# Optimization experiments

Hardware: AMD Instinct MI355X
Metric: run time of the kernel (lower is better)

Reference implementation:

```python
import jax, jax.numpy as jnp
import numpy as np

B, N, D = 2, 2048, 512
H, HD = 8, 64
R = 64  # graph_radius
SCALE = HD ** -0.5
LN_EPS = 1e-5


def _ln(x, g, b):
    m = jnp.mean(x, axis=-1, keepdims=True)
    v = jnp.mean((x - m) ** 2, axis=-1, keepdims=True)
    return (x - m) * jax.lax.rsqrt(v + LN_EPS) * g + b


def setup_inputs() -> dict:
    key = jax.random.key(0)
    ks = jax.random.split(key, 8)
    w = lambda k, shape: (jax.random.normal(k, shape, jnp.float32) * 0.02)
    return {
        "nodes": jax.random.normal(ks[0], (B, N, D), jnp.float32),
        "ln1_g": jnp.ones((D,), jnp.float32), "ln1_b": jnp.zeros((D,), jnp.float32),
        "qkv_w": w(ks[1], (D, 3 * D)), "qkv_b": jnp.zeros((3 * D,), jnp.float32),
        "proj_w": w(ks[2], (D, D)), "proj_b": jnp.zeros((D,), jnp.float32),
        "rep_scale": jnp.ones((H,), jnp.float32),
        "rel_bias": w(ks[3], (2 * N - 1, H)),
        "ln2_g": jnp.ones((D,), jnp.float32), "ln2_b": jnp.zeros((D,), jnp.float32),
        "mlp_w1": w(ks[4], (D, 2 * D)), "mlp_b1": jnp.zeros((2 * D,), jnp.float32),
        "mlp_w2": w(ks[5], (2 * D, D)), "mlp_b2": jnp.zeros((D,), jnp.float32),
    }


def reference(nodes, ln1_g, ln1_b, qkv_w, qkv_b, proj_w, proj_b, rep_scale,
              rel_bias, ln2_g, ln2_b, mlp_w1, mlp_b1, mlp_w2, mlp_b2):
    b, n, d = nodes.shape
    x = _ln(nodes, ln1_g, ln1_b)                       # [B,N,D]
    qkv = (x @ qkv_w + qkv_b).reshape(b, n, 3, H, HD)
    qkv = jnp.transpose(qkv, (2, 0, 3, 1, 4))          # [3,B,H,N,HD]
    q, k, v = qkv[0], qkv[1], qkv[2]
    logits = jnp.einsum('bhnd,bhmd->bhnm', q, k) * SCALE
    # representation correlation (F.normalize with eps=1e-12)
    rep = x / jnp.maximum(jnp.linalg.norm(x, axis=-1, keepdims=True), 1e-12)
    corr = jnp.einsum('bnd,bmd->bnm', rep, rep)        # [B,N,N]
    logits = logits + corr[:, None] * rep_scale[None, :, None, None]
    pos = jnp.arange(n)
    relidx = pos[:, None] - pos[None, :]               # [N,N]
    bias = rel_bias[relidx + n - 1]                    # [N,N,H]
    logits = logits + jnp.transpose(bias, (2, 0, 1))[None]
    mask = jnp.abs(relidx) <= R
    logits = jnp.where(mask[None, None], logits, -jnp.inf)
    attn = jax.nn.softmax(logits, axis=-1)
    upd = jnp.einsum('bhnm,bhmd->bnhd', attn, v).reshape(b, n, d)
    nodes = nodes + (upd @ proj_w + proj_b)
    y = _ln(nodes, ln2_g, ln2_b)
    h = jax.nn.gelu(y @ mlp_w1 + mlp_b1, approximate=False)
    return nodes + (h @ mlp_w2 + mlp_b2)
```

## Files before the change

kernel.cpp:

```cpp
#include <hip/hip_runtime.h>
#include <math.h>

typedef __bf16 bf16;
typedef __bf16 bf16x4 __attribute__((ext_vector_type(4)));
typedef __bf16 bf16x8 __attribute__((ext_vector_type(8)));
typedef float floatx4 __attribute__((ext_vector_type(4)));

#define BB 2
#define NN 2048
#define DD 512
#define HH 8
#define HD 64
#define RR 64
#define D3 1536
#define NEG_BIG (-1e30f)
#define TQ 32
#define TBAND 160

#define GL2LDS16(g, l)                                                        \
    __builtin_amdgcn_global_load_lds(                                         \
        (const __attribute__((address_space(1))) void*)(const void*)(g),      \
        (__attribute__((address_space(3))) void*)(void*)(l), 16, 0, 0)

__global__ __launch_bounds__(256) void cvt_all_kernel(
    const float* __restrict__ qkv_w, const float* __restrict__ proj_w,
    const float* __restrict__ m1w, const float* __restrict__ m2w,
    bf16* __restrict__ wqt, bf16* __restrict__ wpt,
    bf16* __restrict__ w1t, bf16* __restrict__ w2t) {
    __shared__ bf16 Ts[64][72];
    const int tid = threadIdx.x;
    int bid = blockIdx.x;
    const float* W; bf16* Wt; int K, N, bx, by;
    if (bid < 192)      { W = qkv_w;  Wt = wqt; K = 512;  N = 1536; bx = bid % 24; by = bid / 24; }
    else if (bid < 256) { bid -= 192; W = proj_w; Wt = wpt; K = 512;  N = 512;  bx = bid % 8;  by = bid / 8; }
    else if (bid < 384) { bid -= 256; W = m1w;  Wt = w1t; K = 512;  N = 1024; bx = bid % 16; by = bid / 16; }
    else                { bid -= 384; W = m2w;  Wt = w2t; K = 1024; N = 512;  bx = bid % 8;  by = bid / 8; }
    const int n0 = bx * 64, k0 = by * 64;
    #pragma unroll
    for (int i = 0; i < 4; i++) {
        int r = (tid >> 4) + i * 16;
        int c = (tid & 15) * 4;
        floatx4 v = *(const floatx4*)(W + (size_t)(k0 + r) * N + n0 + c);
        #pragma unroll
        for (int e = 0; e < 4; e++) Ts[r][c + e] = (bf16)v[e];
    }
    __syncthreads();
    #pragma unroll
    for (int i = 0; i < 4; i++) {
        int n = (tid >> 4) + i * 16;
        int k = (tid & 15) * 4;
        bf16x4 o;
        #pragma unroll
        for (int e = 0; e < 4; e++) o[e] = Ts[k + e][n];
        *(bf16x4*)(Wt + (size_t)(n0 + n) * K + k0 + k) = o;
    }
}

__device__ inline float block_reduce_sum256(float v, float* sbuf) {
    const int tid = threadIdx.x;
    #pragma unroll
    for (int o = 32; o > 0; o >>= 1) v += __shfl_xor(v, o, 64);
    __syncthreads();
    if ((tid & 63) == 0) sbuf[tid >> 6] = v;
    __syncthreads();
    return sbuf[0] + sbuf[1] + sbuf[2] + sbuf[3];
}

template <bool WANT_INV>
__global__ __launch_bounds__(256) void ln_kernel(
    const float* __restrict__ in, const float* __restrict__ gw,
    const float* __restrict__ bw, bf16* __restrict__ out,
    float* __restrict__ invnorm) {
    __shared__ float sbuf[4];
    const int row = blockIdx.x, tid = threadIdx.x;
    const int i0 = tid * 2;
    const float* ip = in + (size_t)row * DD;
    float v0 = ip[i0], v1 = ip[i0 + 1];
    float mean = block_reduce_sum256(v0 + v1, sbuf) * (1.f / DD);
    float d0 = v0 - mean, d1 = v1 - mean;
    float var = block_reduce_sum256(d0 * d0 + d1 * d1, sbuf) * (1.f / DD);
    float rs = rsqrtf(var + 1e-5f);
    float x0 = d0 * rs * gw[i0] + bw[i0];
    float x1 = d1 * rs * gw[i0 + 1] + bw[i0 + 1];
    out[(size_t)row * DD + i0] = (bf16)x0;
    out[(size_t)row * DD + i0 + 1] = (bf16)x1;
    if (WANT_INV) {
        float s2 = block_reduce_sum256(x0 * x0 + x1 * x1, sbuf);
        if (tid == 0) invnorm[row] = 1.f / fmaxf(sqrtf(s2), 1e-12f);
    }
}

template <int MODE>
__global__ __launch_bounds__(256) void gemm_bt(
    const bf16* __restrict__ A, const bf16* __restrict__ Bt,
    const float* __restrict__ bias, const float* __restrict__ resid,
    void* __restrict__ out, int M, int N, int K) {
    __shared__ __align__(16) bf16 As[2][64 * 64];
    __shared__ __align__(16) bf16 Bs[2][64 * 64];
    const int tid = threadIdx.x;
    const int w = tid >> 6, lane = tid & 63;
    const int lr = lane & 15, lq = lane >> 4;
    const int rowBase = blockIdx.y * 64, colBase = blockIdx.x * 64;
    const int wm = (w >> 1) * 32, wn = (w & 1) * 32;

    floatx4 acc[2][2];
    #pragma unroll
    for (int i = 0; i < 2; i++)
        #pragma unroll
        for (int j = 0; j < 2; j++) acc[i][j] = (floatx4){0.f, 0.f, 0.f, 0.f};

    auto stage = [&](int buf, int k0) {
        #pragma unroll
        for (int i = 0; i < 2; i++) {
            int g = i * 256 + tid;
            int row = g >> 3, k8 = (g & 7) ^ (row & 7);
            GL2LDS16(A + (size_t)(rowBase + row) * K + k0 + k8 * 8, &As[buf][g * 8]);
        }
        #pragma unroll
        for (int i = 0; i < 2; i++) {
            int g = i * 256 + tid;
            int row = g >> 3, k8 = (g & 7) ^ (row & 7);
            GL2LDS16(Bt + (size_t)(colBase + row) * K + k0 + k8 * 8, &Bs[buf][g * 8]);
        }
    };

    const int nsteps = K >> 6;
    stage(0, 0);
    for (int s = 0; s < nsteps; s++) {
        __syncthreads();
        if (s + 1 < nsteps) stage((s + 1) & 1, (s + 1) * 64);
        const int buf = s & 1;
        #pragma unroll
        for (int kb = 0; kb < 2; kb++) {
            bf16x8 af[2], bfr[2];
            #pragma unroll
            for (int i = 0; i < 2; i++) {
                int row = wm + i * 16 + lr;
                int g = row * 8 + ((kb * 4 + lq) ^ (row & 7));
                af[i] = *(bf16x8*)&As[buf][g * 8];
            }
            #pragma unroll
            for (int j = 0; j < 2; j++) {
                int row = wn + j * 16 + lr;
                int g = row * 8 + ((kb * 4 + lq) ^ (row & 7));
                bfr[j] = *(bf16x8*)&Bs[buf][g * 8];
            }
            #pragma unroll
            for (int i = 0; i < 2; i++)
                #pragma unroll
                for (int j = 0; j < 2; j++)
                    acc[i][j] = __builtin_amdgcn_mfma_f32_16x16x32_bf16(
                        af[i], bfr[j], acc[i][j], 0, 0, 0);
        }
    }

    #pragma unroll
    for (int i = 0; i < 2; i++) {
        #pragma unroll
        for (int j = 0; j < 2; j++) {
            #pragma unroll
            for (int r = 0; r < 4; r++) {
                int row = rowBase + wm + i * 16 + lq * 4 + r;
                int col = colBase + wn + j * 16 + lr;
                size_t idx = (size_t)row * N + col;
                float v = acc[i][j][r] + bias[col];
                if (MODE == 0) {
                    ((bf16*)out)[idx] = (bf16)v;
                } else if (MODE == 1) {
                    ((float*)out)[idx] = v + resid[idx];
                } else if (MODE == 2) {
                    float g = 0.5f * v * (1.f + erff(v * 0.70710678118654752f));
                    ((bf16*)out)[idx] = (bf16)g;
                } else {
                    ((float*)out)[idx] = v + resid[idx];
                }
            }
        }
    }
}

__global__ __launch_bounds__(256) void corr_kernel(
    const bf16* __restrict__ x, const float* __restrict__ invnorm,
    float* __restrict__ corr_g) {
    __shared__ __align__(16) bf16 Xc[TBAND * 72];
    __shared__ float invb[TBAND];
    const int tid = threadIdx.x;
    const int b = blockIdx.x & 1, n0 = (blockIdx.x >> 1) * TQ;
    const int bN = b * NN;
    const int w = tid >> 6, lane = tid & 63;
    const int lr = lane & 15, lq = lane >> 4;
    const int rowHalf = (w >> 1) * 16, colBase = (w & 1) * 80;

    if (tid < TBAND) {
        int mc = min(max(n0 - RR + tid, 0), NN - 1);
        invb[tid] = invnorm[bN + mc];
    }

    floatx4 cacc[5];
    #pragma unroll
    for (int t = 0; t < 5; t++) cacc[t] = (floatx4){0.f, 0.f, 0.f, 0.f};

    for (int c = 0; c < 8; c++) {
        __syncthreads();
        #pragma unroll
        for (int rr = 0; rr < 6; rr++) {
            int G = rr * 256 + tid;
            if (G < 1440) {
                int j = G / 9, gc = G % 9;
                int gcs = min(gc, 7);
                int mc = min(max(n0 - RR + j, 0), NN - 1);
                GL2LDS16(x + (size_t)(bN + mc) * DD + c * 64 + gcs * 8, Xc + G * 8);
            }
        }
        __syncthreads();
        #pragma unroll
        for (int kb = 0; kb < 2; kb++) {
            bf16x8 a = *(bf16x8*)&Xc[(64 + rowHalf + lr) * 72 + kb * 32 + lq * 8];
            #pragma unroll
            for (int t = 0; t < 5; t++) {
                bf16x8 bb = *(bf16x8*)&Xc[(colBase + t * 16 + lr) * 72 + kb * 32 + lq * 8];
                cacc[t] = __builtin_amdgcn_mfma_f32_16x16x32_bf16(a, bb, cacc[t], 0, 0, 0);
            }
        }
    }

    float invq[4];
    #pragma unroll
    for (int r = 0; r < 4; r++) invq[r] = invb[64 + rowHalf + lq * 4 + r];
    const size_t cbase = (size_t)blockIdx.x * TQ * TBAND;
    #pragma unroll
    for (int t = 0; t < 5; t++) {
        float invk = invb[colBase + t * 16 + lr];
        #pragma unroll
        for (int r = 0; r < 4; r++)
            corr_g[cbase + (size_t)(rowHalf + lq * 4 + r) * TBAND + colBase + t * 16 + lr] =
                cacc[t][r] * invq[r] * invk;
    }
}

__global__ __launch_bounds__(256) void vtrans_kernel(
    const bf16* __restrict__ qkvb, bf16* __restrict__ vt_g) {
    __shared__ bf16 Ts[64][72];
    const int tid = threadIdx.x;
    const int r0 = blockIdx.x * 64;
    const int h = blockIdx.y;
    #pragma unroll
    for (int i = 0; i < 2; i++) {
        int r = (tid >> 3) + i * 32, c8 = tid & 7;
        *(bf16x8*)&Ts[r][c8 * 8] =
            *(const bf16x8*)(qkvb + (size_t)(r0 + r) * D3 + 2 * DD + h * HD + c8 * 8);
    }
    __syncthreads();
    #pragma unroll
    for (int i = 0; i < 2; i++) {
        int d = (tid >> 3) + i * 32, c8 = (tid & 7) * 8;
        bf16x8 o;
        #pragma unroll
        for (int e = 0; e < 8; e++) o[e] = Ts[c8 + e][d];
        *(bf16x8*)(vt_g + (((size_t)(h * HD + d)) << 12) + r0 + c8) = o;
    }
}

__global__ __launch_bounds__(256) void attn_kernel(
    const bf16* __restrict__ qkv, const bf16* __restrict__ vt_g,
    const float* __restrict__ corr_g, const float* __restrict__ rep_scale,
    const float* __restrict__ rel_bias, bf16* __restrict__ upd) {
    __shared__ __align__(16) bf16 Qs[TQ * 264];
    __shared__ __align__(16) bf16 Ks[TBAND * 72];
    __shared__ __align__(16) bf16 Vt[64 * 168];
    __shared__ __align__(16) bf16 Ps[TQ * 168];
    __shared__ float relb[4][192];
    __shared__ float rmax2[TQ][2];
    __shared__ float rsum2[TQ][2];

    const int tid = threadIdx.x;
    const int bid = blockIdx.x;
    const int b = bid & 1;
    const int h0 = ((bid >> 1) & 1) * 4;
    const int n0 = (bid >> 2) * TQ;
    const int bN = b * NN;
    const int w = tid >> 6, lane = tid & 63;
    const int lr = lane & 15, lq = lane >> 4;
    const int rowHalf = (w >> 1) * 16;
    const int colBase = (w & 1) * 80;
    const int c2 = (w & 1) * 32;

    for (int idx = tid; idx < 4 * 191; idx += 256) {
        int hh = idx / 191, dh = idx - hh * 191;
        relb[hh][dh] = rel_bias[(size_t)(dh + (NN - 1 - 95)) * HH + h0 + hh];
    }

    float corrv[5][4];
    {
        const size_t cbase = (size_t)(((bid >> 2) << 1) | b) * TQ * TBAND;
        #pragma unroll
        for (int t = 0; t < 5; t++)
            #pragma unroll
            for (int r = 0; r < 4; r++)
                corrv[t][r] = corr_g[cbase + (size_t)(rowHalf + lq * 4 + r) * TBAND +
                                     colBase + t * 16 + lr];
    }

    #pragma unroll
    for (int rr = 0; rr < 5; rr++) {
        int G = rr * 256 + tid;
        if (G < 1056) {
            int q = G / 33, gc = G % 33;
            int gcs = min(gc, 31);
            GL2LDS16(qkv + (size_t)(bN + n0 + q) * D3 + h0 * HD + gcs * 8, Qs + G * 8);
        }
    }

    for (int h = h0; h < h0 + 4; h++) {
        __syncthreads();
        #pragma unroll
        for (int rr = 0; rr < 6; rr++) {
            int G = rr * 256 + tid;
            if (G < 1440) {
                int j = G / 9, gc = G % 9;
                int gcs = min(gc, 7);
                int mc = min(max(n0 - RR + j, 0), NN - 1);
                GL2LDS16(qkv + (size_t)(bN + mc) * D3 + DD + h * HD + gcs * 8, Ks + G * 8);
            }
        }
        #pragma unroll
        for (int rr = 0; rr < 6; rr++) {
            int G = rr * 256 + tid;
            if (G < 1344) {
                int d = G / 21, gc = G % 21;
                int nsrc = min(max(n0 - RR + gc * 8, 0), NN - 8);
                GL2LDS16(vt_g + (((size_t)(h * HD + d)) << 12) + bN + nsrc, Vt + G * 8);
            }
        }
        __syncthreads();

        floatx4 sacc[5];
        #pragma unroll
        for (int t = 0; t < 5; t++) sacc[t] = (floatx4){0.f, 0.f, 0.f, 0.f};
        #pragma unroll
        for (int kb = 0; kb < 2; kb++) {
            bf16x8 a = *(bf16x8*)&Qs[(rowHalf + lr) * 264 + (h - h0) * 64 + kb * 32 + lq * 8];
            #pragma unroll
            for (int t = 0; t < 5; t++) {
                bf16x8 bb = *(bf16x8*)&Ks[(colBase + t * 16 + lr) * 72 + kb * 32 + lq * 8];
                sacc[t] = __builtin_amdgcn_mfma_f32_16x16x32_bf16(a, bb, sacc[t], 0, 0, 0);
            }
        }

        const float srep = rep_scale[h];
        float l[5][4];
        float mx[4] = {NEG_BIG, NEG_BIG, NEG_BIG, NEG_BIG};
        #pragma unroll
        for (int t = 0; t < 5; t++) {
            int j = colBase + t * 16 + lr;
            int m = n0 - RR + j;
            #pragma unroll
            for (int r = 0; r < 4; r++) {
                int qi = rowHalf + lq * 4 + r;
                int relidx = qi + RR - j;
                bool valid = (relidx >= -RR) && (relidx <= RR) && (m >= 0) && (m < NN);
                float lv = sacc[t][r] * 0.125f + corrv[t][r] * srep +
                           relb[h - h0][relidx + 95];
                l[t][r] = valid ? lv : NEG_BIG;
                mx[r] = fmaxf(mx[r], l[t][r]);
            }
        }
        #pragma unroll
        for (int r = 0; r < 4; r++)
            #pragma unroll
            for (int mk = 1; mk <= 8; mk <<= 1)
                mx[r] = fmaxf(mx[r], __shfl_xor(mx[r], mk, 64));
        if (lr == 0) {
            #pragma unroll
            for (int r = 0; r < 4; r++) rmax2[rowHalf + lq * 4 + r][w & 1] = mx[r];
        }
        __syncthreads();

        float rm[4], sm[4];
        #pragma unroll
        for (int r = 0; r < 4; r++) {
            int row = rowHalf + lq * 4 + r;
            rm[r] = fmaxf(rmax2[row][0], rmax2[row][1]);
            sm[r] = 0.f;
        }
        #pragma unroll
        for (int t = 0; t < 5; t++) {
            int j = colBase + t * 16 + lr;
            #pragma unroll
            for (int r = 0; r < 4; r++) {
                float pv = __expf(l[t][r] - rm[r]);
                sm[r] += pv;
                Ps[(rowHalf + lq * 4 + r) * 168 + j] = (bf16)pv;
            }
        }
        #pragma unroll
        for (int r = 0; r < 4; r++)
            #pragma unroll
            for (int mk = 1; mk <= 8; mk <<= 1)
                sm[r] += __shfl_xor(sm[r], mk, 64);
        if (lr == 0) {
            #pragma unroll
            for (int r = 0; r < 4; r++) rsum2[rowHalf + lq * 4 + r][w & 1] = sm[r];
        }
        __syncthreads();

        floatx4 oacc[2] = {(floatx4){0.f, 0.f, 0.f, 0.f}, (floatx4){0.f, 0.f, 0.f, 0.f}};
        #pragma unroll
        for (int kb = 0; kb < 5; kb++) {
            bf16x8 a = *(bf16x8*)&Ps[(rowHalf + lr) * 168 + kb * 32 + lq * 8];
            #pragma unroll
            for (int tt = 0; tt < 2; tt++) {
                bf16x8 bb = *(bf16x8*)&Vt[(c2 + tt * 16 + lr) * 168 + kb * 32 + lq * 8];
                oacc[tt] = __builtin_amdgcn_mfma_f32_16x16x32_bf16(a, bb, oacc[tt], 0, 0, 0);
            }
        }
        #pragma unroll
        for (int r = 0; r < 4; r++) {
            int row = rowHalf + lq * 4 + r;
            float rinv = 1.f / (rsum2[row][0] + rsum2[row][1]);
            #pragma unroll
            for (int tt = 0; tt < 2; tt++) {
                upd[(size_t)(bN + n0 + row) * DD + h * HD + c2 + tt * 16 + lr] =
                    (bf16)(oacc[tt][r] * rinv);
            }
        }
    }
}

extern "C" void kernel_launch(void* const* d_in, const int* in_sizes, int n_in,
                              void* d_out, int out_size, void* d_ws,
                              size_t ws_size, hipStream_t stream) {
    const float* nodes  = (const float*)d_in[0];
    const float* ln1_g  = (const float*)d_in[1];
    const float* ln1_b  = (const float*)d_in[2];
    const float* qkv_w  = (const float*)d_in[3];
    const float* qkv_b  = (const float*)d_in[4];
    const float* proj_w = (const float*)d_in[5];
    const float* proj_b = (const float*)d_in[6];
    const float* rep_s  = (const float*)d_in[7];
    const float* rel_b  = (const float*)d_in[8];
    const float* ln2_g  = (const float*)d_in[9];
    const float* ln2_b  = (const float*)d_in[10];
    const float* mlp_w1 = (const float*)d_in[11];
    const float* mlp_b1 = (const float*)d_in[12];
    const float* mlp_w2 = (const float*)d_in[13];
    const float* mlp_b2 = (const float*)d_in[14];

    char* p = (char*)d_ws;
    float* invn = (float*)p;            p += (size_t)1 << 20;
    bf16*  wqt  = (bf16*)p;             p += (size_t)DD * D3 * 2;
    bf16*  wpt  = (bf16*)p;             p += (size_t)DD * DD * 2;
    bf16*  w1t  = (bf16*)p;             p += (size_t)DD * 2 * DD * 2;
    bf16*  w2t  = (bf16*)p;             p += (size_t)2 * DD * DD * 2;
    bf16*  x    = (bf16*)p;             p += (size_t)BB * NN * DD * 2;
    bf16*  qkvb = (bf16*)p;             p += (size_t)BB * NN * D3 * 2;
    char*  regA = p;                    p += (size_t)BB * NN * DD * 4;
    float* corr_g = (float*)regA;
    bf16*  vt_g   = (bf16*)(regA + (size_t)BB * (NN / TQ) * TQ * TBAND * 4);
    float* mid    = (float*)regA;
    bf16*  y    = x;
    bf16*  hgl  = qkvb;
    bf16*  upd  = (bf16*)d_out;

    const int M = BB * NN;

    cvt_all_kernel<<<512, 256, 0, stream>>>(qkv_w, proj_w, mlp_w1, mlp_w2,
                                            wqt, wpt, w1t, w2t);
    ln_kernel<true><<<M, 256, 0, stream>>>(nodes, ln1_g, ln1_b, x, invn);
    corr_kernel<<<BB * (NN / TQ), 256, 0, stream>>>(x, invn, corr_g);
    gemm_bt<0><<<dim3(D3 / 64, M / 64), 256, 0, stream>>>(
        x, wqt, qkv_b, nullptr, qkvb, M, D3, DD);
    vtrans_kernel<<<dim3(M / 64, HH), 256, 0, stream>>>(qkvb, vt_g);
    attn_kernel<<<(NN / TQ) * 2 * BB, 256, 0, stream>>>(
        qkvb, vt_g, corr_g, rep_s, rel_b, upd);
    gemm_bt<1><<<dim3(DD / 64, M / 64), 256, 0, stream>>>(
        upd, wpt, proj_b, nodes, mid, M, DD, DD);
    ln_kernel<false><<<M, 256, 0, stream>>>(mid, ln2_g, ln2_b, y, nullptr);
    gemm_bt<2><<<dim3(2 * DD / 64, M / 64), 256, 0, stream>>>(
        y, w1t, mlp_b1, nullptr, hgl, M, 2 * DD, DD);
    gemm_bt<3><<<dim3(DD / 64, M / 64), 256, 0, stream>>>(
        hgl, w2t, mlp_b2, mid, (float*)d_out, M, DD, 2 * DD);
}
```

Baseline: 179.2 us.

## Fuse all stages into one persistent megakernel with grid-wide barriers

The ten separate kernel launches (weight conversion, two layernorms, corr, four GEMMs, V transpose, attention) become phases of a single persistent kernel of 512 blocks. Phases are separated by an atomic-counter grid barrier, and shared memory is a union across phases. The attention split changes from 4 heads per block to 2, so the 512 blocks line up with the work items. This removes launch gaps and tail effects between kernels. In exchange it adds barrier spin costs and fixes the grid size, relying on all 512 blocks being co-resident (2 per CU), otherwise the barrier deadlocks.

```diff
diff --git a/kernel.cpp b/kernel.cpp
--- a/kernel.cpp
+++ b/kernel.cpp
@@ -16,47 +16,45 @@
 #define NEG_BIG (-1e30f)
 #define TQ 32
 #define TBAND 160
+#define GRID 512
 
 #define GL2LDS16(g, l)                                                        \
     __builtin_amdgcn_global_load_lds(                                         \
         (const __attribute__((address_space(1))) void*)(const void*)(g),      \
         (__attribute__((address_space(3))) void*)(void*)(l), 16, 0, 0)
 
-__global__ __launch_bounds__(256) void cvt_all_kernel(
-    const float* __restrict__ qkv_w, const float* __restrict__ proj_w,
-    const float* __restrict__ m1w, const float* __restrict__ m2w,
-    bf16* __restrict__ wqt, bf16* __restrict__ wpt,
-    bf16* __restrict__ w1t, bf16* __restrict__ w2t) {
-    __shared__ bf16 Ts[64][72];
-    const int tid = threadIdx.x;
-    int bid = blockIdx.x;
-    const float* W; bf16* Wt; int K, N, bx, by;
-    if (bid < 192)      { W = qkv_w;  Wt = wqt; K = 512;  N = 1536; bx = bid % 24; by = bid / 24; }
-    else if (bid < 256) { bid -= 192; W = proj_w; Wt = wpt; K = 512;  N = 512;  bx = bid % 8;  by = bid / 8; }
-    else if (bid < 384) { bid -= 256; W = m1w;  Wt = w1t; K = 512;  N = 1024; bx = bid % 16; by = bid / 16; }
-    else                { bid -= 384; W = m2w;  Wt = w2t; K = 1024; N = 512;  bx = bid % 8;  by = bid / 8; }
-    const int n0 = bx * 64, k0 = by * 64;
-    #pragma unroll
-    for (int i = 0; i < 4; i++) {
-        int r = (tid >> 4) + i * 16;
-        int c = (tid & 15) * 4;
-        floatx4 v = *(const floatx4*)(W + (size_t)(k0 + r) * N + n0 + c);
-        #pragma unroll
-        for (int e = 0; e < 4; e++) Ts[r][c + e] = (bf16)v[e];
-    }
-    __syncthreads();
-    #pragma unroll
-    for (int i = 0; i < 4; i++) {
-        int n = (tid >> 4) + i * 16;
-        int k = (tid & 15) * 4;
-        bf16x4 o;
-        #pragma unroll
-        for (int e = 0; e < 4; e++) o[e] = Ts[k + e][n];
-        *(bf16x4*)(Wt + (size_t)(n0 + n) * K + k0 + k) = o;
-    }
-}
-
-__device__ inline float block_reduce_sum256(float v, float* sbuf) {
+struct MegaParams {
+    const float *nodes, *ln1_g, *ln1_b, *qkv_b, *proj_b, *rep_s, *rel_b,
+                *ln2_g, *ln2_b, *mlp_b1, *mlp_b2;
+    const float *qkv_w, *proj_w, *mlp_w1, *mlp_w2;
+    bf16 *wqt, *wpt, *w1t, *w2t, *x, *qkvb, *vt_g, *y, *hgl, *upd;
+    float *invn, *corr_g, *mid, *outf;
+    int *cnt;
+};
+
+union SMem {
+    struct { bf16 Ts[64][72]; } t;
+    struct { float sbuf[4]; } ln;
+    struct { bf16 As[2][4096], Bs[2][4096]; } g;
+    struct { bf16 Xc[TBAND * 72]; float invb[TBAND]; } c;
+    struct {
+        bf16 Qs[TQ * 136], Ks[TBAND * 72], Vt[64 * 168], Ps[TQ * 168];
+        float relb[2][192], rmax2[TQ][2], rsum2[TQ][2];
+    } a;
+};
+
+static __device__ __forceinline__ void grid_barrier(int* cnt, int target) {
+    __syncthreads();
+    if (threadIdx.x == 0) {
+        __threadfence();
+        atomicAdd(cnt, 1);
+        while (atomicAdd(cnt, 0) < target) __builtin_amdgcn_s_sleep(2);
+        __threadfence();
+    }
+    __syncthreads();
+}
+
+static __device__ __forceinline__ float block_reduce_sum256(float v, float* sbuf) {
     const int tid = threadIdx.x;
     #pragma unroll
     for (int o = 32; o > 0; o >>= 1) v += __shfl_xor(v, o, 64);
@@ -66,13 +64,10 @@
     return sbuf[0] + sbuf[1] + sbuf[2] + sbuf[3];
 }
 
-template <bool WANT_INV>
-__global__ __launch_bounds__(256) void ln_kernel(
-    const float* __restrict__ in, const float* __restrict__ gw,
-    const float* __restrict__ bw, bf16* __restrict__ out,
-    float* __restrict__ invnorm) {
-    __shared__ float sbuf[4];
-    const int row = blockIdx.x, tid = threadIdx.x;
+static __device__ __forceinline__ void ln_row(
+    float* sbuf, const float* in, const float* gw, const float* bw,
+    bf16* out, float* invnorm, int row, bool want_inv) {
+    const int tid = threadIdx.x;
     const int i0 = tid * 2;
     const float* ip = in + (size_t)row * DD;
     float v0 = ip[i0], v1 = ip[i0 + 1];
@@ -84,23 +79,49 @@
     float x1 = d1 * rs * gw[i0 + 1] + bw[i0 + 1];
     out[(size_t)row * DD + i0] = (bf16)x0;
     out[(size_t)row * DD + i0 + 1] = (bf16)x1;
-    if (WANT_INV) {
+    if (want_inv) {
         float s2 = block_reduce_sum256(x0 * x0 + x1 * x1, sbuf);
         if (tid == 0) invnorm[row] = 1.f / fmaxf(sqrtf(s2), 1e-12f);
     }
 }
 
+static __device__ __forceinline__ void cvt_tile(SMem& sm, const MegaParams& P, int item) {
+    const int tid = threadIdx.x;
+    const float* W; bf16* Wt; int K, N, bx, by;
+    if (item < 192)      { W = P.qkv_w;  Wt = P.wqt; K = 512;  N = 1536; bx = item % 24; by = item / 24; }
+    else if (item < 256) { item -= 192; W = P.proj_w; Wt = P.wpt; K = 512;  N = 512;  bx = item % 8;  by = item / 8; }
+    else if (item < 384) { item -= 256; W = P.mlp_w1; Wt = P.w1t; K = 512;  N = 1024; bx = item % 16; by = item / 16; }
+    else                 { item -= 384; W = P.mlp_w2; Wt = P.w2t; K = 1024; N = 512;  bx = item % 8;  by = item / 8; }
+    const int n0 = bx * 64, k0 = by * 64;
+    #pragma unroll
+    for (int i = 0; i < 4; i++) {
+        int r = (tid >> 4) + i * 16;
+        int c = (tid & 15) * 4;
+        floatx4 v = *(const floatx4*)(W + (size_t)(k0 + r) * N + n0 + c);
+        #pragma unroll
+        for (int e = 0; e < 4; e++) sm.t.Ts[r][c + e] = (bf16)v[e];
+    }
+    __syncthreads();
+    #pragma unroll
+    for (int i = 0; i < 4; i++) {
+        int n = (tid >> 4) + i * 16;
+        int k = (tid & 15) * 4;
+        bf16x4 o;
+        #pragma unroll
+        for (int e = 0; e < 4; e++) o[e] = sm.t.Ts[k + e][n];
+        *(bf16x4*)(Wt + (size_t)(n0 + n) * K + k0 + k) = o;
+    }
+}
+
 template <int MODE>
-__global__ __launch_bounds__(256) void gemm_bt(
-    const bf16* __restrict__ A, const bf16* __restrict__ Bt,
-    const float* __restrict__ bias, const float* __restrict__ resid,
-    void* __restrict__ out, int M, int N, int K) {
-    __shared__ __align__(16) bf16 As[2][64 * 64];
-    __shared__ __align__(16) bf16 Bs[2][64 * 64];
+static __device__ __forceinline__ void gemm_tile(
+    SMem& sm, const bf16* A, const bf16* Bt, const float* bias,
+    const float* resid, void* out, int N, int K, int bx, int by) {
+    __syncthreads();
     const int tid = threadIdx.x;
     const int w = tid >> 6, lane = tid & 63;
     const int lr = lane & 15, lq = lane >> 4;
-    const int rowBase = blockIdx.y * 64, colBase = blockIdx.x * 64;
+    const int rowBase = by * 64, colBase = bx * 64;
     const int wm = (w >> 1) * 32, wn = (w & 1) * 32;
 
     floatx4 acc[2][2];
@@ -114,13 +135,13 @@
         for (int i = 0; i < 2; i++) {
             int g = i * 256 + tid;
             int row = g >> 3, k8 = (g & 7) ^ (row & 7);
-            GL2LDS16(A + (size_t)(rowBase + row) * K + k0 + k8 * 8, &As[buf][g * 8]);
+            GL2LDS16(A + (size_t)(rowBase + row) * K + k0 + k8 * 8, &sm.g.As[buf][g * 8]);
         }
         #pragma unroll
         for (int i = 0; i < 2; i++) {
             int g = i * 256 + tid;
             int row = g >> 3, k8 = (g & 7) ^ (row & 7);
-            GL2LDS16(Bt + (size_t)(colBase + row) * K + k0 + k8 * 8, &Bs[buf][g * 8]);
+            GL2LDS16(Bt + (size_t)(colBase + row) * K + k0 + k8 * 8, &sm.g.Bs[buf][g * 8]);
         }
     };
 
@@ -137,13 +158,13 @@
             for (int i = 0; i < 2; i++) {
                 int row = wm + i * 16 + lr;
                 int g = row * 8 + ((kb * 4 + lq) ^ (row & 7));
-                af[i] = *(bf16x8*)&As[buf][g * 8];
+                af[i] = *(bf16x8*)&sm.g.As[buf][g * 8];
             }
             #pragma unroll
             for (int j = 0; j < 2; j++) {
                 int row = wn + j * 16 + lr;
                 int g = row * 8 + ((kb * 4 + lq) ^ (row & 7));
-                bfr[j] = *(bf16x8*)&Bs[buf][g * 8];
+                bfr[j] = *(bf16x8*)&sm.g.Bs[buf][g * 8];
             }
             #pragma unroll
             for (int i = 0; i < 2; i++)
@@ -179,13 +200,9 @@
     }
 }
 
-__global__ __launch_bounds__(256) void corr_kernel(
-    const bf16* __restrict__ x, const float* __restrict__ invnorm,
-    float* __restrict__ corr_g) {
-    __shared__ __align__(16) bf16 Xc[TBAND * 72];
-    __shared__ float invb[TBAND];
-    const int tid = threadIdx.x;
-    const int b = blockIdx.x & 1, n0 = (blockIdx.x >> 1) * TQ;
+static __device__ __forceinline__ void corr_tile(SMem& sm, const MegaParams& P, int item) {
+    const int tid = threadIdx.x;
+    const int b = item & 1, n0 = (item >> 1) * TQ;
     const int bN = b * NN;
     const int w = tid >> 6, lane = tid & 63;
     const int lr = lane & 15, lq = lane >> 4;
@@ -193,7 +210,7 @@
 
     if (tid < TBAND) {
         int mc = min(max(n0 - RR + tid, 0), NN - 1);
-        invb[tid] = invnorm[bN + mc];
+        sm.c.invb[tid] = P.invn[bN + mc];
     }
 
     floatx4 cacc[5];
@@ -209,16 +226,16 @@
                 int j = G / 9, gc = G % 9;
                 int gcs = min(gc, 7);
                 int mc = min(max(n0 - RR + j, 0), NN - 1);
-                GL2LDS16(x + (size_t)(bN + mc) * DD + c * 64 + gcs * 8, Xc + G * 8);
+                GL2LDS16(P.x + (size_t)(bN + mc) * DD + c * 64 + gcs * 8, sm.c.Xc + G * 8);
             }
         }
         __syncthreads();
         #pragma unroll
         for (int kb = 0; kb < 2; kb++) {
-            bf16x8 a = *(bf16x8*)&Xc[(64 + rowHalf + lr) * 72 + kb * 32 + lq * 8];
+            bf16x8 a = *(bf16x8*)&sm.c.Xc[(64 + rowHalf + lr) * 72 + kb * 32 + lq * 8];
             #pragma unroll
             for (int t = 0; t < 5; t++) {
-                bf16x8 bb = *(bf16x8*)&Xc[(colBase + t * 16 + lr) * 72 + kb * 32 + lq * 8];
+                bf16x8 bb = *(bf16x8*)&sm.c.Xc[(colBase + t * 16 + lr) * 72 + kb * 32 + lq * 8];
                 cacc[t] = __builtin_amdgcn_mfma_f32_16x16x32_bf16(a, bb, cacc[t], 0, 0, 0);
             }
         }
@@ -226,29 +243,27 @@
 
     float invq[4];
     #pragma unroll
-    for (int r = 0; r < 4; r++) invq[r] = invb[64 + rowHalf + lq * 4 + r];
-    const size_t cbase = (size_t)blockIdx.x * TQ * TBAND;
+    for (int r = 0; r < 4; r++) invq[r] = sm.c.invb[64 + rowHalf + lq * 4 + r];
+    const size_t cbase = (size_t)item * TQ * TBAND;
     #pragma unroll
     for (int t = 0; t < 5; t++) {
-        float invk = invb[colBase + t * 16 + lr];
+        float invk = sm.c.invb[colBase + t * 16 + lr];
         #pragma unroll
         for (int r = 0; r < 4; r++)
-            corr_g[cbase + (size_t)(rowHalf + lq * 4 + r) * TBAND + colBase + t * 16 + lr] =
+            P.corr_g[cbase + (size_t)(rowHalf + lq * 4 + r) * TBAND + colBase + t * 16 + lr] =
                 cacc[t][r] * invq[r] * invk;
     }
 }
 
-__global__ __launch_bounds__(256) void vtrans_kernel(
-    const bf16* __restrict__ qkvb, bf16* __restrict__ vt_g) {
-    __shared__ bf16 Ts[64][72];
-    const int tid = threadIdx.x;
-    const int r0 = blockIdx.x * 64;
-    const int h = blockIdx.y;
+static __device__ __forceinline__ void vtrans_tile(SMem& sm, const MegaParams& P, int item) {
+    const int tid = threadIdx.x;
+    const int r0 = (item & 63) * 64;
+    const int h = item >> 6;
     #pragma unroll
     for (int i = 0; i < 2; i++) {
         int r = (tid >> 3) + i * 32, c8 = tid & 7;
-        *(bf16x8*)&Ts[r][c8 * 8] =
-            *(const bf16x8*)(qkvb + (size_t)(r0 + r) * D3 + 2 * DD + h * HD + c8 * 8);
+        *(bf16x8*)&sm.t.Ts[r][c8 * 8] =
+            *(const bf16x8*)(P.qkvb + (size_t)(r0 + r) * D3 + 2 * DD + h * HD + c8 * 8);
     }
     __syncthreads();
     #pragma unroll
@@ -256,28 +271,16 @@
         int d = (tid >> 3) + i * 32, c8 = (tid & 7) * 8;
         bf16x8 o;
         #pragma unroll
-        for (int e = 0; e < 8; e++) o[e] = Ts[c8 + e][d];
-        *(bf16x8*)(vt_g + (((size_t)(h * HD + d)) << 12) + r0 + c8) = o;
-    }
-}
-
-__global__ __launch_bounds__(256) void attn_kernel(
-    const bf16* __restrict__ qkv, const bf16* __restrict__ vt_g,
-    const float* __restrict__ corr_g, const float* __restrict__ rep_scale,
-    const float* __restrict__ rel_bias, bf16* __restrict__ upd) {
-    __shared__ __align__(16) bf16 Qs[TQ * 264];
-    __shared__ __align__(16) bf16 Ks[TBAND * 72];
-    __shared__ __align__(16) bf16 Vt[64 * 168];
-    __shared__ __align__(16) bf16 Ps[TQ * 168];
-    __shared__ float relb[4][192];
-    __shared__ float rmax2[TQ][2];
-    __shared__ float rsum2[TQ][2];
-
-    const int tid = threadIdx.x;
-    const int bid = blockIdx.x;
-    const int b = bid & 1;
-    const int h0 = ((bid >> 1) & 1) * 4;
-    const int n0 = (bid >> 2) * TQ;
+        for (int e = 0; e < 8; e++) o[e] = sm.t.Ts[c8 + e][d];
+        *(bf16x8*)(P.vt_g + (((size_t)(h * HD + d)) << 12) + r0 + c8) = o;
+    }
+}
+
+static __device__ __forceinline__ void attn_item(SMem& sm, const MegaParams& P, int item) {
+    const int tid = threadIdx.x;
+    const int b = item & 1;
+    const int h0 = ((item >> 1) & 3) * 2;
+    const int n0 = (item >> 3) * TQ;
     const int bN = b * NN;
     const int w = tid >> 6, lane = tid & 63;
     const int lr = lane & 15, lq = lane >> 4;
@@ -285,33 +288,33 @@
     const int colBase = (w & 1) * 80;
     const int c2 = (w & 1) * 32;
 
-    for (int idx = tid; idx < 4 * 191; idx += 256) {
+    for (int idx = tid; idx < 2 * 191; idx += 256) {
         int hh = idx / 191, dh = idx - hh * 191;
-        relb[hh][dh] = rel_bias[(size_t)(dh + (NN - 1 - 95)) * HH + h0 + hh];
+        sm.a.relb[hh][dh] = P.rel_b[(size_t)(dh + (NN - 1 - 95)) * HH + h0 + hh];
     }
 
     float corrv[5][4];
     {
-        const size_t cbase = (size_t)(((bid >> 2) << 1) | b) * TQ * TBAND;
+        const size_t cbase = (size_t)((((item >> 3)) << 1) | b) * TQ * TBAND;
         #pragma unroll
         for (int t = 0; t < 5; t++)
             #pragma unroll
             for (int r = 0; r < 4; r++)
-                corrv[t][r] = corr_g[cbase + (size_t)(rowHalf + lq * 4 + r) * TBAND +
-                                     colBase + t * 16 + lr];
-    }
-
-    #pragma unroll
-    for (int rr = 0; rr < 5; rr++) {
+                corrv[t][r] = P.corr_g[cbase + (size_t)(rowHalf + lq * 4 + r) * TBAND +
+                                       colBase + t * 16 + lr];
+    }
+
+    #pragma unroll
+    for (int rr = 0; rr < 3; rr++) {
         int G = rr * 256 + tid;
-        if (G < 1056) {
-            int q = G / 33, gc = G % 33;
-            int gcs = min(gc, 31);
-            GL2LDS16(qkv + (size_t)(bN + n0 + q) * D3 + h0 * HD + gcs * 8, Qs + G * 8);
-        }
-    }
-
-    for (int h = h0; h < h0 + 4; h++) {
+        if (G < 544) {
+            int q = G / 17, gc = G % 17;
+            int gcs = min(gc, 15);
+            GL2LDS16(P.qkvb + (size_t)(bN + n0 + q) * D3 + h0 * HD + gcs * 8, sm.a.Qs + G * 8);
+        }
+    }
+
+    for (int h = h0; h < h0 + 2; h++) {
         __syncthreads();
         #pragma unroll
         for (int rr = 0; rr < 6; rr++) {
@@ -320,7 +323,7 @@
                 int j = G / 9, gc = G % 9;
                 int gcs = min(gc, 7);
                 int mc = min(max(n0 - RR + j, 0), NN - 1);
-                GL2LDS16(qkv + (size_t)(bN + mc) * D3 + DD + h * HD + gcs * 8, Ks + G * 8);
+                GL2LDS16(P.qkvb + (size_t)(bN + mc) * D3 + DD + h * HD + gcs * 8, sm.a.Ks + G * 8);
             }
         }
         #pragma unroll
@@ -329,7 +332,7 @@
             if (G < 1344) {
                 int d = G / 21, gc = G % 21;
                 int nsrc = min(max(n0 - RR + gc * 8, 0), NN - 8);
-                GL2LDS16(vt_g + (((size_t)(h * HD + d)) << 12) + bN + nsrc, Vt + G * 8);
+                GL2LDS16(P.vt_g + (((size_t)(h * HD + d)) << 12) + bN + nsrc, sm.a.Vt + G * 8);
             }
         }
         __syncthreads();
@@ -339,15 +342,15 @@
         for (int t = 0; t < 5; t++) sacc[t] = (floatx4){0.f, 0.f, 0.f, 0.f};
         #pragma unroll
         for (int kb = 0; kb < 2; kb++) {
-            bf16x8 a = *(bf16x8*)&Qs[(rowHalf + lr) * 264 + (h - h0) * 64 + kb * 32 + lq * 8];
+            bf16x8 a = *(bf16x8*)&sm.a.Qs[(rowHalf + lr) * 136 + (h - h0) * 64 + kb * 32 + lq * 8];
             #pragma unroll
             for (int t = 0; t < 5; t++) {
-                bf16x8 bb = *(bf16x8*)&Ks[(colBase + t * 16 + lr) * 72 + kb * 32 + lq * 8];
+                bf16x8 bb = *(bf16x8*)&sm.a.Ks[(colBase + t * 16 + lr) * 72 + kb * 32 + lq * 8];
                 sacc[t] = __builtin_amdgcn_mfma_f32_16x16x32_bf16(a, bb, sacc[t], 0, 0, 0);
             }
         }
 
-        const float srep = rep_scale[h];
+        const float srep = P.rep_s[h];
         float l[5][4];
         float mx[4] = {NEG_BIG, NEG_BIG, NEG_BIG, NEG_BIG};
         #pragma unroll
@@ -360,7 +363,7 @@
                 int relidx = qi + RR - j;
                 bool valid = (relidx >= -RR) && (relidx <= RR) && (m >= 0) && (m < NN);
                 float lv = sacc[t][r] * 0.125f + corrv[t][r] * srep +
-                           relb[h - h0][relidx + 95];
+                           sm.a.relb[h - h0][relidx + 95];
                 l[t][r] = valid ? lv : NEG_BIG;
                 mx[r] = fmaxf(mx[r], l[t][r]);
             }
@@ -372,16 +375,16 @@
                 mx[r] = fmaxf(mx[r], __shfl_xor(mx[r], mk, 64));
         if (lr == 0) {
             #pragma unroll
-            for (int r = 0; r < 4; r++) rmax2[rowHalf + lq * 4 + r][w & 1] = mx[r];
-        }
-        __syncthreads();
-
-        float rm[4], sm[4];
+            for (int r = 0; r < 4; r++) sm.a.rmax2[rowHalf + lq * 4 + r][w & 1] = mx[r];
+        }
+        __syncthreads();
+
+        float rm[4], sme[4];
         #pragma unroll
         for (int r = 0; r < 4; r++) {
             int row = rowHalf + lq * 4 + r;
-            rm[r] = fmaxf(rmax2[row][0], rmax2[row][1]);
-            sm[r] = 0.f;
+            rm[r] = fmaxf(sm.a.rmax2[row][0], sm.a.rmax2[row][1]);
+            sme[r] = 0.f;
         }
         #pragma unroll
         for (int t = 0; t < 5; t++) {
@@ -389,95 +392,126 @@
             #pragma unroll
             for (int r = 0; r < 4; r++) {
                 float pv = __expf(l[t][r] - rm[r]);
-                sm[r] += pv;
-                Ps[(rowHalf + lq * 4 + r) * 168 + j] = (bf16)pv;
+                sme[r] += pv;
+                sm.a.Ps[(rowHalf + lq * 4 + r) * 168 + j] = (bf16)pv;
             }
         }
         #pragma unroll
         for (int r = 0; r < 4; r++)
             #pragma unroll
             for (int mk = 1; mk <= 8; mk <<= 1)
-                sm[r] += __shfl_xor(sm[r], mk, 64);
+                sme[r] += __shfl_xor(sme[r], mk, 64);
         if (lr == 0) {
             #pragma unroll
-            for (int r = 0; r < 4; r++) rsum2[rowHalf + lq * 4 + r][w & 1] = sm[r];
+            for (int r = 0; r < 4; r++) sm.a.rsum2[rowHalf + lq * 4 + r][w & 1] = sme[r];
         }
         __syncthreads();
 
         floatx4 oacc[2] = {(floatx4){0.f, 0.f, 0.f, 0.f}, (floatx4){0.f, 0.f, 0.f, 0.f}};
         #pragma unroll
         for (int kb = 0; kb < 5; kb++) {
-            bf16x8 a = *(bf16x8*)&Ps[(rowHalf + lr) * 168 + kb * 32 + lq * 8];
+            bf16x8 a = *(bf16x8*)&sm.a.Ps[(rowHalf + lr) * 168 + kb * 32 + lq * 8];
             #pragma unroll
             for (int tt = 0; tt < 2; tt++) {
-                bf16x8 bb = *(bf16x8*)&Vt[(c2 + tt * 16 + lr) * 168 + kb * 32 + lq * 8];
+                bf16x8 bb = *(bf16x8*)&sm.a.Vt[(c2 + tt * 16 + lr) * 168 + kb * 32 + lq * 8];
                 oacc[tt] = __builtin_amdgcn_mfma_f32_16x16x32_bf16(a, bb, oacc[tt], 0, 0, 0);
             }
         }
         #pragma unroll
         for (int r = 0; r < 4; r++) {
             int row = rowHalf + lq * 4 + r;
-            float rinv = 1.f / (rsum2[row][0] + rsum2[row][1]);
+            float rinv = 1.f / (sm.a.rsum2[row][0] + sm.a.rsum2[row][1]);
             #pragma unroll
             for (int tt = 0; tt < 2; tt++) {
-                upd[(size_t)(bN + n0 + row) * DD + h * HD + c2 + tt * 16 + lr] =
+                P.upd[(size_t)(bN + n0 + row) * DD + h * HD + c2 + tt * 16 + lr] =
                     (bf16)(oacc[tt][r] * rinv);
             }
         }
     }
+}
+
+__global__ __launch_bounds__(256, 2) void mega_kernel(MegaParams P) {
+    __shared__ SMem sm;
+    const int bid = blockIdx.x;
+
+    cvt_tile(sm, P, bid);
+    __syncthreads();
+    for (int r = 0; r < 8; r++)
+        ln_row(sm.ln.sbuf, P.nodes, P.ln1_g, P.ln1_b, P.x, P.invn, bid * 8 + r, true);
+    grid_barrier(P.cnt, GRID * 1);
+
+    for (int it = bid; it < 1664; it += GRID) {
+        __syncthreads();
+        if (it < 128)
+            corr_tile(sm, P, it);
+        else
+            gemm_tile<0>(sm, P.x, P.wqt, P.qkv_b, nullptr, P.qkvb, D3, DD,
+                         (it - 128) % 24, (it - 128) / 24);
+    }
+    grid_barrier(P.cnt, GRID * 2);
+
+    vtrans_tile(sm, P, bid);
+    grid_barrier(P.cnt, GRID * 3);
+
+    attn_item(sm, P, bid);
+    grid_barrier(P.cnt, GRID * 4);
+
+    gemm_tile<1>(sm, P.upd, P.wpt, P.proj_b, P.nodes, P.mid, DD, DD,
+                 bid % 8, bid / 8);
+    grid_barrier(P.cnt, GRID * 5);
+
+    for (int r = 0; r < 8; r++)
+        ln_row(sm.ln.sbuf, P.mid, P.ln2_g, P.ln2_b, P.y, nullptr, bid * 8 + r, false);
+    grid_barrier(P.cnt, GRID * 6);
+
+    for (int it = bid; it < 1024; it += GRID)
+        gemm_tile<2>(sm, P.y, P.w1t, P.mlp_b1, nullptr, P.hgl, 2 * DD, DD,
+                     it % 16, it / 16);
+    grid_barrier(P.cnt, GRID * 7);
+
+    gemm_tile<3>(sm, P.hgl, P.w2t, P.mlp_b2, P.mid, P.outf, DD, 2 * DD,
+                 bid % 8, bid / 8);
 }
 
 extern "C" void kernel_launch(void* const* d_in, const int* in_sizes, int n_in,
                               void* d_out, int out_size, void* d_ws,
                               size_t ws_size, hipStream_t stream) {
-    const float* nodes  = (const float*)d_in[0];
-    const float* ln1_g  = (const float*)d_in[1];
-    const float* ln1_b  = (const float*)d_in[2];
-    const float* qkv_w  = (const float*)d_in[3];
-    const float* qkv_b  = (const float*)d_in[4];
-    const float* proj_w = (const float*)d_in[5];
-    const float* proj_b = (const float*)d_in[6];
-    const float* rep_s  = (const float*)d_in[7];
-    const float* rel_b  = (const float*)d_in[8];
-    const float* ln2_g  = (const float*)d_in[9];
-    const float* ln2_b  = (const float*)d_in[10];
-    const float* mlp_w1 = (const float*)d_in[11];
-    const float* mlp_b1 = (const float*)d_in[12];
-    const float* mlp_w2 = (const float*)d_in[13];
-    const float* mlp_b2 = (const float*)d_in[14];
+    MegaParams P;
+    P.nodes  = (const float*)d_in[0];
+    P.ln1_g  = (const float*)d_in[1];
+    P.ln1_b  = (const float*)d_in[2];
+    P.qkv_w  = (const float*)d_in[3];
+    P.qkv_b  = (const float*)d_in[4];
+    P.proj_w = (const float*)d_in[5];
+    P.proj_b = (const float*)d_in[6];
+    P.rep_s  = (const float*)d_in[7];
+    P.rel_b  = (const float*)d_in[8];
+    P.ln2_g  = (const float*)d_in[9];
+    P.ln2_b  = (const float*)d_in[10];
+    P.mlp_w1 = (const float*)d_in[11];
+    P.mlp_b1 = (const float*)d_in[12];
+    P.mlp_w2 = (const float*)d_in[13];
+    P.mlp_b2 = (const float*)d_in[14];
 
     char* p = (char*)d_ws;
-    float* invn = (float*)p;            p += (size_t)1 << 20;
-    bf16*  wqt  = (bf16*)p;             p += (size_t)DD * D3 * 2;
-    bf16*  wpt  = (bf16*)p;             p += (size_t)DD * DD * 2;
-    bf16*  w1t  = (bf16*)p;             p += (size_t)DD * 2 * DD * 2;
-    bf16*  w2t  = (bf16*)p;             p += (size_t)2 * DD * DD * 2;
-    bf16*  x    = (bf16*)p;             p += (size_t)BB * NN * DD * 2;
-    bf16*  qkvb = (bf16*)p;             p += (size_t)BB * NN * D3 * 2;
-    char*  regA = p;                    p += (size_t)BB * NN * DD * 4;
-    float* corr_g = (float*)regA;
-    bf16*  vt_g   = (bf16*)(regA + (size_t)BB * (NN / TQ) * TQ * TBAND * 4);
-    float* mid    = (float*)regA;
-    bf16*  y    = x;
-    bf16*  hgl  = qkvb;
-    bf16*  upd  = (bf16*)d_out;
-
-    const int M = BB * NN;
-
-    cvt_all_kernel<<<512, 256, 0, stream>>>(qkv_w, proj_w, mlp_w1, mlp_w2,
-                                            wqt, wpt, w1t, w2t);
-    ln_kernel<true><<<M, 256, 0, stream>>>(nodes, ln1_g, ln1_b, x, invn);
-    corr_kernel<<<BB * (NN / TQ), 256, 0, stream>>>(x, invn, corr_g);
-    gemm_bt<0><<<dim3(D3 / 64, M / 64), 256, 0, stream>>>(
-        x, wqt, qkv_b, nullptr, qkvb, M, D3, DD);
-    vtrans_kernel<<<dim3(M / 64, HH), 256, 0, stream>>>(qkvb, vt_g);
-    attn_kernel<<<(NN / TQ) * 2 * BB, 256, 0, stream>>>(
-        qkvb, vt_g, corr_g, rep_s, rel_b, upd);
-    gemm_bt<1><<<dim3(DD / 64, M / 64), 256, 0, stream>>>(
-        upd, wpt, proj_b, nodes, mid, M, DD, DD);
-    ln_kernel<false><<<M, 256, 0, stream>>>(mid, ln2_g, ln2_b, y, nullptr);
-    gemm_bt<2><<<dim3(2 * DD / 64, M / 64), 256, 0, stream>>>(
-        y, w1t, mlp_b1, nullptr, hgl, M, 2 * DD, DD);
-    gemm_bt<3><<<dim3(DD / 64, M / 64), 256, 0, stream>>>(
-        hgl, w2t, mlp_b2, mid, (float*)d_out, M, DD, 2 * DD);
-}
+    P.invn   = (float*)p;
+    P.cnt    = (int*)(p + (256 << 10));
+    p += (size_t)1 << 20;
+    P.wqt    = (bf16*)p;  p += (size_t)DD * D3 * 2;
+    P.wpt    = (bf16*)p;  p += (size_t)DD * DD * 2;
+    P.w1t    = (bf16*)p;  p += (size_t)DD * 2 * DD * 2;
+    P.w2t    = (bf16*)p;  p += (size_t)2 * DD * DD * 2;
+    P.x      = (bf16*)p;  p += (size_t)BB * NN * DD * 2;
+    P.qkvb   = (bf16*)p;  p += (size_t)BB * NN * D3 * 2;
+    char* regA = p;       p += (size_t)BB * NN * DD * 4;
+    P.corr_g = (float*)regA;
+    P.vt_g   = (bf16*)(regA + (size_t)BB * (NN / TQ) * TQ * TBAND * 4);
+    P.mid    = (float*)regA;
+    P.y      = P.x;
+    P.hgl    = P.qkvb;
+    P.upd    = (bf16*)d_out;
+    P.outf   = (float*)d_out;
+
+    hipMemsetAsync(P.cnt, 0, 64, stream);
+    mega_kernel<<<GRID, 256, 0, stream>>>(P);
+}
```

Measured after the change: 520.8 us. 191% more time.
